# Kernel optimization log

Hardware: AMD Instinct MI355X
Metric: run time of the kernel (lower is better)

## Reference

```python
import jax, jax.numpy as jnp
import numpy as np

D_MODEL = 1024
H = 16
D_K = D_MODEL // H
B = 2
S = 2048
NEG = -1000000000.0


def setup_inputs() -> dict:
    key = jax.random.key(0)
    ks = jax.random.split(key, 11)
    sc = 1.0 / np.sqrt(D_MODEL)
    inp = {
        "q": jax.random.normal(ks[0], (B, S, D_MODEL), jnp.float32),
        "k": jax.random.normal(ks[1], (B, S, D_MODEL), jnp.float32),
        "v": jax.random.normal(ks[2], (B, S, D_MODEL), jnp.float32),
        "mask": jnp.tril(jnp.ones((S, S), jnp.int32))[None, None, :, :],  # causal [1,1,S,S]
        "Wq": jax.random.normal(ks[3], (D_MODEL, D_MODEL), jnp.float32) * sc,
        "bq": jnp.zeros((D_MODEL,), jnp.float32),
        "Wk": jax.random.normal(ks[4], (D_MODEL, D_MODEL), jnp.float32) * sc,
        "bk": jnp.zeros((D_MODEL,), jnp.float32),
        "Wv": jax.random.normal(ks[5], (D_MODEL, D_MODEL), jnp.float32) * sc,
        "bv": jnp.zeros((D_MODEL,), jnp.float32),
        "Wo": jax.random.normal(ks[6], (D_MODEL, D_MODEL), jnp.float32) * sc,
        "bo": jnp.zeros((D_MODEL,), jnp.float32),
    }
    return inp


def reference(q, k, v, mask, Wq, bq, Wk, bk, Wv, bv, Wo, bo):
    # Linear projections (torch Linear: x @ W.T + b)
    query = q @ Wq.T + bq
    key_ = k @ Wk.T + bk
    value = v @ Wv.T + bv
    # [B,S,D] -> [B,H,S,Dk]
    def split_heads(x):
        return x.reshape(B, S, H, D_K).transpose(0, 2, 1, 3)
    query, key_, value = split_heads(query), split_heads(key_), split_heads(value)
    # scaled dot-product attention, scores [B,H,S,S]
    scores = jnp.einsum("bhqd,bhkd->bhqk", query, key_) / jnp.sqrt(
        jnp.asarray(D_K, query.dtype))
    scores = jnp.where(mask == 0, jnp.asarray(NEG, scores.dtype), scores)
    attn = jax.nn.softmax(scores, axis=-1)
    x = jnp.einsum("bhqk,bhkd->bhqd", attn, value)
    # merge heads [B,H,S,Dk] -> [B,S,D]
    x = x.transpose(0, 2, 1, 3).reshape(B, S, D_MODEL)
    return x @ Wo.T + bo
```

## Files before the change

### kernel.cpp

```cpp
#include <hip/hip_runtime.h>
#include <stdint.h>

#define D_MODEL 1024
#define NHEAD   16
#define DKH     64
#define NB      2
#define SSEQ    2048

typedef unsigned short u16;
typedef __bf16 bf16x8 __attribute__((ext_vector_type(8)));
typedef float  f32x4  __attribute__((ext_vector_type(4)));
typedef float  f32x16 __attribute__((ext_vector_type(16)));
typedef u16    u16x8  __attribute__((ext_vector_type(8)));

__device__ __forceinline__ u16 f2bf(float x) {
  union { float f; uint32_t u; } c; c.f = x;
  uint32_t r = c.u + 0x7FFFu + ((c.u >> 16) & 1u);
  return (u16)(r >> 16);
}

__device__ __forceinline__ uint32_t cvtpk(float lo, float hi) {
  uint32_t r;
  asm("v_cvt_pk_bf16_f32 %0, %1, %2" : "=v"(r) : "v"(lo), "v"(hi));
  return r;
}

__device__ __forceinline__ void gload_lds16(const void* gsrc, void* ldsdst) {
  typedef const __attribute__((address_space(1))) uint32_t* gp_t;
  typedef __attribute__((address_space(3))) uint32_t* lp_t;
  gp_t g = reinterpret_cast<gp_t>(reinterpret_cast<uintptr_t>(gsrc));
  lp_t l = reinterpret_cast<lp_t>(reinterpret_cast<uintptr_t>(ldsdst));
  __builtin_amdgcn_global_load_lds(g, l, 16, 0, 0);
}

__device__ __forceinline__ f32x4 mfma16(bf16x8 a, bf16x8 b, f32x4 c) {
  return __builtin_amdgcn_mfma_f32_16x16x32_bf16(a, b, c, 0, 0, 0);
}
__device__ __forceinline__ f32x16 mfma32(bf16x8 a, bf16x8 b, f32x16 c) {
  return __builtin_amdgcn_mfma_f32_32x32x16_bf16(a, b, c, 0, 0, 0);
}

__device__ __forceinline__ bf16x8 lds_frag(const u16* tile, int row, int kelem) {
  int chunk = (kelem >> 3) ^ (row & 7);
  return *reinterpret_cast<const bf16x8*>(
      reinterpret_cast<const char*>(tile) + row * 128 + chunk * 16);
}

template<int NROWS>
__device__ __forceinline__ void stage_tile(const u16* __restrict__ g, int row0, int ldk,
                                           int k0, u16* ldsbase, int wid, int lane) {
  constexpr int CPW = NROWS / 32;
  #pragma unroll
  for (int i = 0; i < CPW; ++i) {
    int c = wid * CPW + i;
    int row = c * 8 + (lane >> 3);
    int cchunk = (lane & 7) ^ (lane >> 3);
    const u16* src = g + (size_t)(row0 + row) * ldk + k0 + cchunk * 8;
    gload_lds16(src, reinterpret_cast<char*>(ldsbase) + c * 1024);
  }
}

__global__ __launch_bounds__(256) void cast_kernel(
    const float* __restrict__ s0, const float* __restrict__ s1,
    const float* __restrict__ s2, const float* __restrict__ s3,
    u16* __restrict__ d0, u16* __restrict__ d1, u16* __restrict__ d2, u16* __restrict__ d3,
    int n8) {
  const int z = blockIdx.z;
  const float* s = (z == 0) ? s0 : (z == 1) ? s1 : (z == 2) ? s2 : s3;
  u16* d = (z == 0) ? d0 : (z == 1) ? d1 : (z == 2) ? d2 : d3;
  int i = blockIdx.x * 256 + threadIdx.x;
  if (i >= n8) return;
  float4 a = reinterpret_cast<const float4*>(s)[2 * i];
  float4 b = reinterpret_cast<const float4*>(s)[2 * i + 1];
  u16x8 o;
  o[0] = f2bf(a.x); o[1] = f2bf(a.y); o[2] = f2bf(a.z); o[3] = f2bf(a.w);
  o[4] = f2bf(b.x); o[5] = f2bf(b.y); o[6] = f2bf(b.z); o[7] = f2bf(b.w);
  reinterpret_cast<u16x8*>(d)[i] = o;
}

__device__ __forceinline__ void gemm_core(const u16* __restrict__ A, const u16* __restrict__ W,
                                          u16* ldsA, u16* ldsB, int brow, int bcol,
                                          f32x4 acc[4][4]) {
  const int tid = threadIdx.x;
  const int lane = tid & 63;
  const int wid = tid >> 6;
  const int wr = wid >> 1;
  const int wc = wid & 1;
  f32x4 z4 = {0.f, 0.f, 0.f, 0.f};
  #pragma unroll
  for (int i = 0; i < 4; ++i)
    #pragma unroll
    for (int j = 0; j < 4; ++j) acc[i][j] = z4;

  stage_tile<128>(A, brow, D_MODEL, 0, ldsA, wid, lane);
  stage_tile<128>(W, bcol, D_MODEL, 0, ldsB, wid, lane);
  __syncthreads();
  int buf = 0;
  const int KT = D_MODEL / 64;
  for (int kt = 0; kt < KT; ++kt) {
    if (kt + 1 < KT) {
      stage_tile<128>(A, brow, D_MODEL, (kt + 1) * 64, ldsA + (buf ^ 1) * 8192, wid, lane);
      stage_tile<128>(W, bcol, D_MODEL, (kt + 1) * 64, ldsB + (buf ^ 1) * 8192, wid, lane);
    }
    const u16* tA = ldsA + buf * 8192;
    const u16* tB = ldsB + buf * 8192;
    #pragma unroll
    for (int kk = 0; kk < 2; ++kk) {
      const int ke = kk * 32 + ((lane >> 4) << 3);
      bf16x8 af[4], bf[4];
      #pragma unroll
      for (int i = 0; i < 4; ++i) af[i] = lds_frag(tA, wr * 64 + i * 16 + (lane & 15), ke);
      #pragma unroll
      for (int j = 0; j < 4; ++j) bf[j] = lds_frag(tB, wc * 64 + j * 16 + (lane & 15), ke);
      __builtin_amdgcn_s_setprio(1);
      #pragma unroll
      for (int i = 0; i < 4; ++i)
        #pragma unroll
        for (int j = 0; j < 4; ++j) acc[i][j] = mfma16(af[i], bf[j], acc[i][j]);
      __builtin_amdgcn_s_setprio(0);
    }
    __syncthreads();
    buf ^= 1;
  }
}

__global__ __launch_bounds__(256) void gemm_qkv(
    const u16* __restrict__ x0, const u16* __restrict__ x1, const u16* __restrict__ x2,
    const u16* __restrict__ w0, const u16* __restrict__ w1, const u16* __restrict__ w2,
    const float* __restrict__ b0, const float* __restrict__ b1, const float* __restrict__ b2,
    u16* __restrict__ o0, u16* __restrict__ o1, u16* __restrict__ o2) {
  __shared__ u16 ldsA[2 * 128 * 64];
  __shared__ u16 ldsB[2 * 128 * 64];
  const int z = blockIdx.z;
  const u16* X = (z == 0) ? x0 : (z == 1) ? x1 : x2;
  const u16* W = (z == 0) ? w0 : (z == 1) ? w1 : w2;
  const float* bias = (z == 0) ? b0 : (z == 1) ? b1 : b2;
  u16* O = (z == 0) ? o0 : (z == 1) ? o1 : o2;
  const float scale = (z == 0) ? 0.125f : 1.0f;
  const int brow = blockIdx.y * 128;
  const int bcol = blockIdx.x * 128;
  f32x4 acc[4][4];
  gemm_core(X, W, ldsA, ldsB, brow, bcol, acc);
  const int lane = threadIdx.x & 63;
  const int wid = threadIdx.x >> 6;
  const int wr = wid >> 1, wc = wid & 1;
  #pragma unroll
  for (int j = 0; j < 4; ++j) {
    const int n = bcol + wc * 64 + j * 16 + (lane & 15);
    const float bn = bias[n];
    const int h = n >> 6, d = n & 63;
    #pragma unroll
    for (int i = 0; i < 4; ++i)
      #pragma unroll
      for (int r = 0; r < 4; ++r) {
        const int m = brow + wr * 64 + i * 16 + ((lane >> 4) << 2) + r;
        const int bb = m >> 11, s = m & (SSEQ - 1);
        O[(((size_t)(bb * NHEAD + h) * SSEQ + s) << 6) + d] = f2bf((acc[i][j][r] + bn) * scale);
      }
  }
}

__global__ __launch_bounds__(256) void gemm_out(const u16* __restrict__ A,
                                                const u16* __restrict__ W,
                                                const float* __restrict__ bias,
                                                float* __restrict__ out) {
  __shared__ u16 ldsA[2 * 128 * 64];
  __shared__ u16 ldsB[2 * 128 * 64];
  const int brow = blockIdx.y * 128;
  const int bcol = blockIdx.x * 128;
  f32x4 acc[4][4];
  gemm_core(A, W, ldsA, ldsB, brow, bcol, acc);
  const int lane = threadIdx.x & 63;
  const int wid = threadIdx.x >> 6;
  const int wr = wid >> 1, wc = wid & 1;
  #pragma unroll
  for (int j = 0; j < 4; ++j) {
    const int n = bcol + wc * 64 + j * 16 + (lane & 15);
    const float bn = bias[n];
    #pragma unroll
    for (int i = 0; i < 4; ++i)
      #pragma unroll
      for (int r = 0; r < 4; ++r) {
        const int m = brow + wr * 64 + i * 16 + ((lane >> 4) << 2) + r;
        out[(size_t)m * D_MODEL + n] = acc[i][j][r] + bn;
      }
  }
}

__global__ __launch_bounds__(256) void transpose_v(const u16* __restrict__ V,
                                                   u16* __restrict__ Vt) {
  __shared__ u16 t[64][72];
  const int tid = threadIdx.x;
  const int bh = blockIdx.y;
  const int s0 = blockIdx.x * 64;
  const u16* Vb = V + ((size_t)bh * SSEQ + s0) * DKH;
  const int row = tid >> 2;
  const int cg = (tid & 3) * 16;
  uint4 a = *reinterpret_cast<const uint4*>(Vb + (size_t)row * DKH + cg);
  uint4 b = *reinterpret_cast<const uint4*>(Vb + (size_t)row * DKH + cg + 8);
  *reinterpret_cast<uint4*>(&t[row][cg]) = a;
  *reinterpret_cast<uint4*>(&t[row][cg + 8]) = b;
  __syncthreads();
  const int d = tid >> 2;
  const int sg = (tid & 3) * 16;
  u16 vals[16];
  #pragma unroll
  for (int j = 0; j < 16; ++j) vals[j] = t[sg + j][d];
  u16* dst = Vt + ((size_t)bh * DKH + d) * SSEQ + s0 + sg;
  *reinterpret_cast<uint4*>(dst) = *reinterpret_cast<uint4*>(&vals[0]);
  *reinterpret_cast<uint4*>(dst + 8) = *reinterpret_cast<uint4*>(&vals[8]);
}

union W4 { uint32_t w[4]; bf16x8 v; };

__device__ __forceinline__ void attn_strip32(const u16* __restrict__ Qb,
                                             const u16* __restrict__ Kb,
                                             const u16* __restrict__ Vb,
                                             u16* __restrict__ ctxb,
                                             int strip, int lane) {
  const int lo = lane & 31;
  const int hi = lane >> 5;
  const int q0 = strip * 32;
  const int nt = strip + 1;

  bf16x8 qf[4];
  const u16* qrow = Qb + (size_t)(q0 + lo) * DKH + hi * 8;
  #pragma unroll
  for (int s = 0; s < 4; ++s) qf[s] = *reinterpret_cast<const bf16x8*>(qrow + s * 16);

  const u16* krow = Kb + (size_t)lo * DKH + hi * 8;
  bf16x8 kf[4];
  #pragma unroll
  for (int s = 0; s < 4; ++s) kf[s] = *reinterpret_cast<const bf16x8*>(krow + s * 16);

  const u16* vrow = Vb + (size_t)lo * SSEQ + hi * 8;
  bf16x8 vf[2][2];
  #pragma unroll
  for (int kh = 0; kh < 2; ++kh)
    #pragma unroll
    for (int db = 0; db < 2; ++db)
      vf[kh][db] = *reinterpret_cast<const bf16x8*>(vrow + db * 32 * SSEQ + kh * 16);

  f32x16 z16 = {};
  f32x16 acc0 = z16, acc1 = z16;
  float m = -1e30f, lsum = 0.f;

  for (int t = 0; t < nt; ++t) {
    f32x16 sf = z16;
    __builtin_amdgcn_s_setprio(1);
    #pragma unroll
    for (int s = 0; s < 4; ++s) sf = mfma32(kf[s], qf[s], sf);
    __builtin_amdgcn_s_setprio(0);
    if (t + 1 < nt) {
      const u16* kn = krow + (size_t)(t + 1) * 32 * DKH;
      #pragma unroll
      for (int s = 0; s < 4; ++s) kf[s] = *reinterpret_cast<const bf16x8*>(kn + s * 16);
    }
    if (t == nt - 1) {
      #pragma unroll
      for (int r = 0; r < 16; ++r) {
        int kvp = (r & 3) + 8 * (r >> 2) + 4 * hi;
        if (kvp > lo) sf[r] = -1e9f;
      }
    }
    float t01 = fmaxf(sf[0], sf[1]),   t23 = fmaxf(sf[2], sf[3]);
    float t45 = fmaxf(sf[4], sf[5]),   t67 = fmaxf(sf[6], sf[7]);
    float t89 = fmaxf(sf[8], sf[9]),   tab = fmaxf(sf[10], sf[11]);
    float tcd = fmaxf(sf[12], sf[13]), tef = fmaxf(sf[14], sf[15]);
    float pm = fmaxf(fmaxf(fmaxf(t01, t23), fmaxf(t45, t67)),
                     fmaxf(fmaxf(t89, tab), fmaxf(tcd, tef)));
    pm = fmaxf(pm, __shfl_xor(pm, 32));
    if (t == 0) {
      m = pm;
    } else if (!__all(pm - m <= 6.0f)) {
      float mn = fmaxf(m, pm);
      float scl = __expf(m - mn);
      lsum *= scl;
      #pragma unroll
      for (int r = 0; r < 16; ++r) {
        int idx = (((r & 3) + 8 * (r >> 2)) << 2) + (hi << 4);
        float sr = __int_as_float(__builtin_amdgcn_ds_bpermute(idx, __float_as_int(scl)));
        acc0[r] *= sr;
        acc1[r] *= sr;
      }
      m = mn;
    }
    float pr[16];
    #pragma unroll
    for (int r = 0; r < 16; ++r) pr[r] = __expf(sf[r] - m);
    float rs = (((pr[0] + pr[1]) + (pr[2] + pr[3])) + ((pr[4] + pr[5]) + (pr[6] + pr[7]))) +
               (((pr[8] + pr[9]) + (pr[10] + pr[11])) + ((pr[12] + pr[13]) + (pr[14] + pr[15])));
    rs += __shfl_xor(rs, 32);
    lsum += rs;
    uint32_t a = cvtpk(pr[0], pr[1]), b = cvtpk(pr[2], pr[3]);
    uint32_t c = cvtpk(pr[4], pr[5]), d = cvtpk(pr[6], pr[7]);
    uint32_t e = cvtpk(pr[8], pr[9]), f = cvtpk(pr[10], pr[11]);
    uint32_t g = cvtpk(pr[12], pr[13]), h = cvtpk(pr[14], pr[15]);
    uint32_t ap = __shfl_xor((int)a, 32), bp = __shfl_xor((int)b, 32);
    uint32_t cp = __shfl_xor((int)c, 32), dp = __shfl_xor((int)d, 32);
    uint32_t ep = __shfl_xor((int)e, 32), fp = __shfl_xor((int)f, 32);
    uint32_t gp = __shfl_xor((int)g, 32), hp = __shfl_xor((int)h, 32);
    W4 pa0, pa1;
    pa0.w[0] = hi ? cp : a;  pa0.w[1] = hi ? dp : b;
    pa0.w[2] = hi ? c : ap;  pa0.w[3] = hi ? d : bp;
    pa1.w[0] = hi ? gp : e;  pa1.w[1] = hi ? hp : f;
    pa1.w[2] = hi ? g : ep;  pa1.w[3] = hi ? h : fp;
    __builtin_amdgcn_s_setprio(1);
    acc0 = mfma32(pa0.v, vf[0][0], acc0);
    acc0 = mfma32(pa1.v, vf[1][0], acc0);
    acc1 = mfma32(pa0.v, vf[0][1], acc1);
    acc1 = mfma32(pa1.v, vf[1][1], acc1);
    __builtin_amdgcn_s_setprio(0);
    if (t + 1 < nt) {
      const u16* vn = vrow + (t + 1) * 32;
      #pragma unroll
      for (int kh = 0; kh < 2; ++kh)
        #pragma unroll
        for (int db = 0; db < 2; ++db)
          vf[kh][db] = *reinterpret_cast<const bf16x8*>(vn + db * 32 * SSEQ + kh * 16);
    }
  }
  float inv = 1.0f / lsum;
  #pragma unroll
  for (int r = 0; r < 16; ++r) {
    int rp = (r & 3) + 8 * (r >> 2) + 4 * hi;
    int idx = (((r & 3) + 8 * (r >> 2)) << 2) + (hi << 4);
    float ir = __int_as_float(__builtin_amdgcn_ds_bpermute(idx, __float_as_int(inv)));
    u16* orow = ctxb + (size_t)(q0 + rp) * D_MODEL;
    orow[lo] = f2bf(acc0[r] * ir);
    orow[32 + lo] = f2bf(acc1[r] * ir);
  }
}

__global__ __launch_bounds__(64) void attn_kernel(const u16* __restrict__ Q,
                                                  const u16* __restrict__ K,
                                                  const u16* __restrict__ Vt,
                                                  u16* __restrict__ ctx) {
  const int lane = threadIdx.x;
  const int bid = blockIdx.x;
  const int j = bid >> 3;
  const int bh = ((bid & 7) << 2) | (j >> 6);
  const int strip = 63 - (j & 63);
  const u16* Qb = Q + (size_t)bh * SSEQ * DKH;
  const u16* Kb = K + (size_t)bh * SSEQ * DKH;
  const u16* Vb = Vt + (size_t)bh * DKH * SSEQ;
  u16* ctxb = ctx + (size_t)(bh >> 4) * SSEQ * D_MODEL + (bh & 15) * DKH;
  attn_strip32(Qb, Kb, Vb, ctxb, strip, lane);
}

extern "C" void kernel_launch(void* const* d_in, const int* in_sizes, int n_in,
                              void* d_out, int out_size, void* d_ws, size_t ws_size,
                              hipStream_t stream) {
  const float* q  = (const float*)d_in[0];
  const float* k  = (const float*)d_in[1];
  const float* v  = (const float*)d_in[2];
  const float* Wq = (const float*)d_in[4];
  const float* bq = (const float*)d_in[5];
  const float* Wk = (const float*)d_in[6];
  const float* bk = (const float*)d_in[7];
  const float* Wv = (const float*)d_in[8];
  const float* bv = (const float*)d_in[9];
  const float* Wo = (const float*)d_in[10];
  const float* bo = (const float*)d_in[11];

  char* ws = (char*)d_ws;
  const size_t SZ_QKV = (size_t)NB * SSEQ * D_MODEL * 2;
  const size_t SZ_W   = (size_t)D_MODEL * D_MODEL * 2;
  u16* qb  = (u16*)(ws);
  u16* kb  = (u16*)(ws + SZ_QKV);
  u16* vb  = (u16*)(ws + 2 * SZ_QKV);
  u16* wqb = (u16*)(ws + 3 * SZ_QKV);
  u16* wkb = (u16*)(ws + 3 * SZ_QKV + SZ_W);
  u16* wvb = (u16*)(ws + 3 * SZ_QKV + 2 * SZ_W);
  u16* wob = (u16*)(ws + 3 * SZ_QKV + 3 * SZ_W);
  u16* Qh  = (u16*)(ws + 3 * SZ_QKV + 4 * SZ_W);
  u16* Kh  = (u16*)(ws + 4 * SZ_QKV + 4 * SZ_W);
  u16* Vh  = (u16*)(ws + 5 * SZ_QKV + 4 * SZ_W);
  u16* Vth = (u16*)(ws + 6 * SZ_QKV + 4 * SZ_W);
  u16* ctx = (u16*)(ws + 7 * SZ_QKV + 4 * SZ_W);

  cast_kernel<<<dim3(2048, 1, 3), 256, 0, stream>>>(
      q, k, v, nullptr, qb, kb, vb, nullptr, (NB * SSEQ * D_MODEL) / 8);
  cast_kernel<<<dim3(512, 1, 4), 256, 0, stream>>>(
      Wq, Wk, Wv, Wo, wqb, wkb, wvb, wob, (D_MODEL * D_MODEL) / 8);
  gemm_qkv<<<dim3(8, 32, 3), 256, 0, stream>>>(qb, kb, vb, wqb, wkb, wvb,
                                               bq, bk, bv, Qh, Kh, Vh);
  transpose_v<<<dim3(SSEQ / 64, NB * NHEAD), 256, 0, stream>>>(Vh, Vth);
  attn_kernel<<<dim3(2048), 64, 0, stream>>>(Qh, Kh, Vth, ctx);
  gemm_out<<<dim3(8, 32), 256, 0, stream>>>(ctx, wob, bo, (float*)d_out);
}
```

Before: 280.0 us.

## Double-buffer K/V tiles in LDS via async global-to-LDS loads

```diff
diff --git a/kernel.cpp b/kernel.cpp
--- a/kernel.cpp
+++ b/kernel.cpp
@@ -211,13 +211,29 @@
   *reinterpret_cast<uint4*>(dst + 8) = *reinterpret_cast<uint4*>(&vals[8]);
 }
 
-union W4 { uint32_t w[4]; bf16x8 v; };
+__device__ __forceinline__ void stage_kv(const u16* __restrict__ Kb,
+                                         const u16* __restrict__ Vb,
+                                         int t, char* kbuf, char* vbuf, int lane) {
+  const u16* ks = Kb + (size_t)t * 32 * DKH;
+  const int krow = lane >> 3;
+  const int kchunk = (lane & 7) ^ krow;
+  #pragma unroll
+  for (int i = 0; i < 4; ++i)
+    gload_lds16(ks + (size_t)(i * 8 + krow) * DKH + kchunk * 8, kbuf + i * 1024);
+  const int vr = lane >> 2;
+  #pragma unroll
+  for (int i = 0; i < 4; ++i) {
+    int vrow = i * 16 + vr;
+    int csrc = ((lane & 3) - (vrow >> 1)) & 3;
+    gload_lds16(Vb + (size_t)vrow * SSEQ + t * 32 + csrc * 8, vbuf + i * 1024);
+  }
+}
 
 __device__ __forceinline__ void attn_strip32(const u16* __restrict__ Qb,
                                              const u16* __restrict__ Kb,
                                              const u16* __restrict__ Vb,
                                              u16* __restrict__ ctxb,
-                                             int strip, int lane) {
+                                             char* lds, int strip, int lane) {
   const int lo = lane & 31;
   const int hi = lane >> 5;
   const int q0 = strip * 32;
@@ -227,35 +243,37 @@
   const u16* qrow = Qb + (size_t)(q0 + lo) * DKH + hi * 8;
   #pragma unroll
   for (int s = 0; s < 4; ++s) qf[s] = *reinterpret_cast<const bf16x8*>(qrow + s * 16);
-
-  const u16* krow = Kb + (size_t)lo * DKH + hi * 8;
-  bf16x8 kf[4];
-  #pragma unroll
-  for (int s = 0; s < 4; ++s) kf[s] = *reinterpret_cast<const bf16x8*>(krow + s * 16);
-
-  const u16* vrow = Vb + (size_t)lo * SSEQ + hi * 8;
-  bf16x8 vf[2][2];
-  #pragma unroll
-  for (int kh = 0; kh < 2; ++kh)
-    #pragma unroll
-    for (int db = 0; db < 2; ++db)
-      vf[kh][db] = *reinterpret_cast<const bf16x8*>(vrow + db * 32 * SSEQ + kh * 16);
+  asm volatile("s_waitcnt vmcnt(0)" ::: "memory");
+  __builtin_amdgcn_sched_barrier(0);
+
+  stage_kv(Kb, Vb, 0, lds, lds + 4096, lane);
 
   f32x16 z16 = {};
   f32x16 acc0 = z16, acc1 = z16;
   float m = -1e30f, lsum = 0.f;
 
   for (int t = 0; t < nt; ++t) {
+    char* kb_l = lds + (t & 1) * 8192;
+    char* vb_l = kb_l + 4096;
+    if (t + 1 < nt) {
+      stage_kv(Kb, Vb, t + 1, lds + ((t + 1) & 1) * 8192, lds + ((t + 1) & 1) * 8192 + 4096, lane);
+      asm volatile("s_waitcnt vmcnt(8)" ::: "memory");
+    } else {
+      asm volatile("s_waitcnt vmcnt(0)" ::: "memory");
+    }
+    __builtin_amdgcn_sched_barrier(0);
+
+    bf16x8 kf[4];
+    #pragma unroll
+    for (int s = 0; s < 4; ++s)
+      kf[s] = *reinterpret_cast<const bf16x8*>(kb_l + lo * 128 + ((((s << 1) | hi) ^ (lo & 7)) << 4));
+
     f32x16 sf = z16;
     __builtin_amdgcn_s_setprio(1);
     #pragma unroll
     for (int s = 0; s < 4; ++s) sf = mfma32(kf[s], qf[s], sf);
     __builtin_amdgcn_s_setprio(0);
-    if (t + 1 < nt) {
-      const u16* kn = krow + (size_t)(t + 1) * 32 * DKH;
-      #pragma unroll
-      for (int s = 0; s < 4; ++s) kf[s] = *reinterpret_cast<const bf16x8*>(kn + s * 16);
-    }
+
     if (t == nt - 1) {
       #pragma unroll
       for (int r = 0; r < 16; ++r) {
@@ -269,11 +287,10 @@
     float tcd = fmaxf(sf[12], sf[13]), tef = fmaxf(sf[14], sf[15]);
     float pm = fmaxf(fmaxf(fmaxf(t01, t23), fmaxf(t45, t67)),
                      fmaxf(fmaxf(t89, tab), fmaxf(tcd, tef)));
-    pm = fmaxf(pm, __shfl_xor(pm, 32));
     if (t == 0) {
-      m = pm;
+      m = fmaxf(pm, __shfl_xor(pm, 32));
     } else if (!__all(pm - m <= 6.0f)) {
-      float mn = fmaxf(m, pm);
+      float mn = fmaxf(fmaxf(pm, __shfl_xor(pm, 32)), m);
       float scl = __expf(m - mn);
       lsum *= scl;
       #pragma unroll
@@ -290,8 +307,8 @@
     for (int r = 0; r < 16; ++r) pr[r] = __expf(sf[r] - m);
     float rs = (((pr[0] + pr[1]) + (pr[2] + pr[3])) + ((pr[4] + pr[5]) + (pr[6] + pr[7]))) +
                (((pr[8] + pr[9]) + (pr[10] + pr[11])) + ((pr[12] + pr[13]) + (pr[14] + pr[15])));
-    rs += __shfl_xor(rs, 32);
     lsum += rs;
+
     uint32_t a = cvtpk(pr[0], pr[1]), b = cvtpk(pr[2], pr[3]);
     uint32_t c = cvtpk(pr[4], pr[5]), d = cvtpk(pr[6], pr[7]);
     uint32_t e = cvtpk(pr[8], pr[9]), f = cvtpk(pr[10], pr[11]);
@@ -300,27 +317,31 @@
     uint32_t cp = __shfl_xor((int)c, 32), dp = __shfl_xor((int)d, 32);
     uint32_t ep = __shfl_xor((int)e, 32), fp = __shfl_xor((int)f, 32);
     uint32_t gp = __shfl_xor((int)g, 32), hp = __shfl_xor((int)h, 32);
-    W4 pa0, pa1;
+    union W4 { uint32_t w[4]; bf16x8 v; } pa0, pa1;
     pa0.w[0] = hi ? cp : a;  pa0.w[1] = hi ? dp : b;
     pa0.w[2] = hi ? c : ap;  pa0.w[3] = hi ? d : bp;
     pa1.w[0] = hi ? gp : e;  pa1.w[1] = hi ? hp : f;
     pa1.w[2] = hi ? g : ep;  pa1.w[3] = hi ? h : fp;
+
+    bf16x8 vf[2][2];
+    #pragma unroll
+    for (int kh = 0; kh < 2; ++kh)
+      #pragma unroll
+      for (int db = 0; db < 2; ++db) {
+        int row = db * 32 + lo;
+        int cc = (((kh << 1) | hi) + (row >> 1)) & 3;
+        vf[kh][db] = *reinterpret_cast<const bf16x8*>(vb_l + row * 64 + (cc << 4));
+      }
     __builtin_amdgcn_s_setprio(1);
     acc0 = mfma32(pa0.v, vf[0][0], acc0);
     acc0 = mfma32(pa1.v, vf[1][0], acc0);
     acc1 = mfma32(pa0.v, vf[0][1], acc1);
     acc1 = mfma32(pa1.v, vf[1][1], acc1);
     __builtin_amdgcn_s_setprio(0);
-    if (t + 1 < nt) {
-      const u16* vn = vrow + (t + 1) * 32;
-      #pragma unroll
-      for (int kh = 0; kh < 2; ++kh)
-        #pragma unroll
-        for (int db = 0; db < 2; ++db)
-          vf[kh][db] = *reinterpret_cast<const bf16x8*>(vn + db * 32 * SSEQ + kh * 16);
-    }
-  }
-  float inv = 1.0f / lsum;
+  }
+
+  float lt = lsum + __shfl_xor(lsum, 32);
+  float inv = 1.0f / lt;
   #pragma unroll
   for (int r = 0; r < 16; ++r) {
     int rp = (r & 3) + 8 * (r >> 2) + 4 * hi;
@@ -336,6 +357,7 @@
                                                   const u16* __restrict__ K,
                                                   const u16* __restrict__ Vt,
                                                   u16* __restrict__ ctx) {
+  __shared__ alignas(128) char lds[16384];
   const int lane = threadIdx.x;
   const int bid = blockIdx.x;
   const int j = bid >> 3;
@@ -345,7 +367,7 @@
   const u16* Kb = K + (size_t)bh * SSEQ * DKH;
   const u16* Vb = Vt + (size_t)bh * DKH * SSEQ;
   u16* ctxb = ctx + (size_t)(bh >> 4) * SSEQ * D_MODEL + (bh & 15) * DKH;
-  attn_strip32(Qb, Kb, Vb, ctxb, strip, lane);
+  attn_strip32(Qb, Kb, Vb, ctxb, lds, strip, lane);
 }
 
 extern "C" void kernel_launch(void* const* d_in, const int* in_sizes, int n_in,
```

After: 260.1 us. -7.1%, faster.
